# Kernel optimization log

Measured on AMD Instinct MI355X. Metric: run time of the kernel, lower is better.

Reference implementation:

```python
import jax, jax.numpy as jnp
import numpy as np

DIM = 192
HEADS = 6
HIDDEN = 384  # int(DIM * 2.0)


def _ln(x, w, b):
    # WithBias LayerNorm over channel dim (torch normalizes last dim of b,(hw),c)
    mu = jnp.mean(x, axis=1, keepdims=True)
    var = jnp.var(x, axis=1, keepdims=True)
    return (x - mu) / jnp.sqrt(var + 1e-5) * w[None, :, None, None] + b[None, :, None, None]


def _conv1x1(x, w):  # w: [O, I, 1, 1]
    return jnp.einsum('bihw,oi->bohw', x, w[:, :, 0, 0])


def _dwconv3(x, w):  # depthwise 3x3, w: [C, 1, 3, 3]
    return jax.lax.conv_general_dilated(
        x, w, window_strides=(1, 1), padding=((1, 1), (1, 1)),
        feature_group_count=x.shape[1],
        dimension_numbers=('NCHW', 'OIHW', 'NCHW'))


def _l2norm(x):  # F.normalize along last axis
    n = jnp.sqrt(jnp.sum(x * x, axis=-1, keepdims=True))
    return x / jnp.maximum(n, 1e-12)


def setup_inputs() -> dict:
    key = jax.random.key(0)
    ks = jax.random.split(key, 16)
    s = 0.02
    d = {}
    d['x'] = jax.random.normal(ks[0], (2, DIM, 128, 128), dtype=jnp.float32)
    d['k_v'] = jax.random.normal(ks[1], (2, 256), dtype=jnp.float32)
    d['ln1_w'] = jnp.ones((DIM,), jnp.float32)
    d['ln1_b'] = jnp.zeros((DIM,), jnp.float32)
    d['temp'] = jnp.ones((HEADS, 1, 1), jnp.float32)
    d['w_kR'] = jax.random.normal(ks[2], (DIM * 3 // 4, 192), jnp.float32) * s
    d['w_kI'] = jax.random.normal(ks[3], (DIM // 4, 64), jnp.float32) * s
    d['w_qR'] = jax.random.normal(ks[4], (DIM, DIM * 3 // 4, 1, 1), jnp.float32) * s
    d['w_qdw'] = jax.random.normal(ks[5], (DIM, 1, 3, 3), jnp.float32) * s
    d['w_kvI'] = jax.random.normal(ks[6], (DIM * 2, DIM // 4, 1, 1), jnp.float32) * s
    d['w_kvdw'] = jax.random.normal(ks[7], (DIM * 2, 1, 3, 3), jnp.float32) * s
    d['w_po'] = jax.random.normal(ks[8], (DIM, DIM, 1, 1), jnp.float32) * s
    d['ln2_w'] = jnp.ones((DIM,), jnp.float32)
    d['ln2_b'] = jnp.zeros((DIM,), jnp.float32)
    d['w_ffk'] = jax.random.normal(ks[9], (DIM, 256), jnp.float32) * s
    d['w_pin'] = jax.random.normal(ks[10], (HIDDEN * 2, DIM, 1, 1), jnp.float32) * s
    d['w_dw'] = jax.random.normal(ks[11], (HIDDEN * 2, 1, 3, 3), jnp.float32) * s
    d['w_pout'] = jax.random.normal(ks[12], (DIM, HIDDEN, 1, 1), jnp.float32) * s
    return d


def reference(x, k_v, ln1_w, ln1_b, temp, w_kR, w_kI, w_qR, w_qdw, w_kvI, w_kvdw,
              w_po, ln2_w, ln2_b, w_ffk, w_pin, w_dw, w_pout):
    b, c, h, w = x.shape
    c3 = c * 3 // 4
    # ---- Rttention on norm1(x) ----
    xn = _ln(x, ln1_w, ln1_b)
    kvr = (k_v[:, :192] @ w_kR.T)[:, :, None, None]   # [b, 3c/4, 1, 1]
    kvi = (k_v[:, 192:] @ w_kI.T)[:, :, None, None]   # [b, c/4, 1, 1]
    x_r = xn[:, :c3] * kvr + xn[:, :c3]
    x_i = xn[:, c3:] * kvi + xn[:, c3:]
    q = _dwconv3(_conv1x1(x_r, w_qR), w_qdw)          # [b, c, h, w]
    kv = _dwconv3(_conv1x1(x_i, w_kvI), w_kvdw)       # [b, 2c, h, w]
    k, v = jnp.split(kv, 2, axis=1)
    rh = lambda t: t.reshape(b, HEADS, c // HEADS, h * w)
    q = _l2norm(rh(q))
    k = _l2norm(rh(k))
    v = rh(v)
    # channel-wise attention: [b, head, c_h, c_h]
    attn = jax.nn.softmax(jnp.einsum('bhcd,bhed->bhce', q, k) * temp[None], axis=-1)
    out = jnp.einsum('bhce,bhed->bhcd', attn, v).reshape(b, c, h, w)
    x = x + _conv1x1(out, w_po)
    # ---- GDFN FeedForward on norm2(x) ----
    xn2 = _ln(x, ln2_w, ln2_b)
    kvf = (k_v @ w_ffk.T)[:, :, None, None]           # [b, c, 1, 1]
    y = xn2 * kvf + xn2
    y = _dwconv3(_conv1x1(y, w_pin), w_dw)            # [b, 2*hidden, h, w]
    y1, y2 = jnp.split(y, 2, axis=1)
    y = jax.nn.gelu(y1, approximate=False) * y2
    x = x + _conv1x1(y, w_pout)
    return (x, k_v)
```

## Files before the change

kernel.cpp:

```cpp
#include <hip/hip_runtime.h>
#include <math.h>

#define HW 16384
#define IMG 128
#define CDIM 192
#define C3 144
#define C4 48
#define NB 2
#define NPX 32768
#define HEADS 6

typedef unsigned short u16;
typedef unsigned int u32;
typedef __attribute__((ext_vector_type(8))) short bf16x8;
typedef __attribute__((ext_vector_type(4))) float f32x4;

__device__ __forceinline__ float bf2f(u16 u) {
    return __uint_as_float(((unsigned int)u) << 16);
}
__device__ __forceinline__ u16 f2bf(float f) {
    unsigned int x = __float_as_uint(f);
    unsigned int r = x + 0x7fffu + ((x >> 16) & 1u);
    return (u16)(r >> 16);
}

static inline float* wsf(void* ws, size_t off) { return (float*)((char*)ws + off); }
static inline u16* wsh(void* ws, size_t off) { return (u16*)((char*)ws + off); }

__global__ void k_setup(const float* __restrict__ kvv, const float* __restrict__ wkR,
                        const float* __restrict__ wkI, const float* __restrict__ wffk,
                        const float* __restrict__ wqR, const float* __restrict__ wkvI,
                        const float* __restrict__ wpo, const float* __restrict__ wpin,
                        const float* __restrict__ wpout,
                        u16* __restrict__ wb, float* __restrict__ sm,
                        float* __restrict__ tail) {
    int t = blockIdx.x * 256 + threadIdx.x;
    if (t < 313344) {
        float v;
        if (t < 30720) {
            int o = t / 160, i = t % 160;
            v = (i < 144) ? wqR[o * 144 + i] : 0.f;
        } else if (t < 55296) {
            int r = t - 30720; int o = r / 64, i = r % 64;
            v = (i < 48) ? wkvI[o * 48 + i] : 0.f;
        } else if (t < 92160) {
            v = wpo[t - 55296];
        } else if (t < 239616) {
            v = wpin[t - 92160];
        } else {
            v = wpout[t - 239616];
        }
        wb[t] = f2bf(v);
    } else if (t < 314112) {
        int r = t - 313344;
        if (r < 288) {
            int b = r / 144, o = r % 144;
            const float* v = kvv + b * 256;
            const float* w = wkR + o * 192;
            float s = 0.f;
            for (int j = 0; j < 192; j++) s += v[j] * w[j];
            sm[r] = s + 1.0f;
        } else if (r < 384) {
            int r2 = r - 288;
            int b = r2 / 48, o = r2 % 48;
            const float* v = kvv + b * 256 + 192;
            const float* w = wkI + o * 64;
            float s = 0.f;
            for (int j = 0; j < 64; j++) s += v[j] * w[j];
            sm[288 + r2] = s + 1.0f;
        } else {
            int r2 = r - 384;
            int b = r2 / 192, o = r2 % 192;
            const float* v = kvv + b * 256;
            const float* w = wffk + o * 256;
            float s = 0.f;
            for (int j = 0; j < 256; j++) s += v[j] * w[j];
            sm[384 + r2] = s + 1.0f;
        }
    } else if (t < 314624) {
        int r = t - 314112;
        tail[r] = kvv[r];
    }
}

template <bool INBF, bool SPLIT>
__global__ __launch_bounds__(256) void k_ln(
    const void* __restrict__ xin,
    const float* __restrict__ lnw, const float* __restrict__ lnb,
    const float* __restrict__ sca, const float* __restrict__ scb,
    u16* __restrict__ outA, u16* __restrict__ outB) {
    __shared__ float red[2][16][16][4];
    __shared__ float mu_s[16][4], rstd_s[16][4];
    int t = threadIdx.x;
    int px4 = t & 15, cg = t >> 4;
    int base = blockIdx.x * 64;
    int b = base >> 14;
    int p = (base & 16383) + px4 * 4;
    float vals[12][4];
    float s[4] = {0.f, 0.f, 0.f, 0.f}, s2[4] = {0.f, 0.f, 0.f, 0.f};
#pragma unroll
    for (int j = 0; j < 12; j++) {
        int c = cg * 12 + j;
        size_t off = ((size_t)(b * CDIM + c)) * HW + p;
        float v[4];
        if (INBF) {
            ushort4 u = *(const ushort4*)((const u16*)xin + off);
            v[0] = bf2f(u.x); v[1] = bf2f(u.y); v[2] = bf2f(u.z); v[3] = bf2f(u.w);
        } else {
            float4 f = *(const float4*)((const float*)xin + off);
            v[0] = f.x; v[1] = f.y; v[2] = f.z; v[3] = f.w;
        }
#pragma unroll
        for (int q = 0; q < 4; q++) {
            vals[j][q] = v[q]; s[q] += v[q]; s2[q] += v[q] * v[q];
        }
    }
#pragma unroll
    for (int q = 0; q < 4; q++) { red[0][cg][px4][q] = s[q]; red[1][cg][px4][q] = s2[q]; }
    __syncthreads();
    if (t < 16) {
        float S[4] = {0.f, 0.f, 0.f, 0.f}, S2[4] = {0.f, 0.f, 0.f, 0.f};
        for (int g2 = 0; g2 < 16; g2++)
#pragma unroll
            for (int q = 0; q < 4; q++) { S[q] += red[0][g2][t][q]; S2[q] += red[1][g2][t][q]; }
#pragma unroll
        for (int q = 0; q < 4; q++) {
            float mu = S[q] * (1.0f / CDIM);
            float var = S2[q] * (1.0f / CDIM) - mu * mu;
            mu_s[t][q] = mu;
            rstd_s[t][q] = rsqrtf(var + 1e-5f);
        }
    }
    __syncthreads();
    float mu[4], rs[4];
#pragma unroll
    for (int q = 0; q < 4; q++) { mu[q] = mu_s[px4][q]; rs[q] = rstd_s[px4][q]; }
#pragma unroll
    for (int j = 0; j < 12; j++) {
        int c = cg * 12 + j;
        float w = lnw[c], bb = lnb[c];
        float sc; u16* op; size_t off;
        if (SPLIT) {
            if (c < C3) { sc = sca[b * C3 + c]; off = ((size_t)(b * C3 + c)) * HW + p; op = outA; }
            else { sc = scb[b * C4 + c - C3]; off = ((size_t)(b * C4 + c - C3)) * HW + p; op = outB; }
        } else {
            sc = sca[b * CDIM + c]; off = ((size_t)(b * CDIM + c)) * HW + p; op = outA;
        }
        ushort4 o;
        o.x = f2bf(((vals[j][0] - mu[0]) * rs[0] * w + bb) * sc);
        o.y = f2bf(((vals[j][1] - mu[1]) * rs[1] * w + bb) * sc);
        o.z = f2bf(((vals[j][2] - mu[2]) * rs[2] * w + bb) * sc);
        o.w = f2bf(((vals[j][3] - mu[3]) * rs[3] * w + bb) * sc);
        *(ushort4*)(op + off) = o;
    }
}

template <int NCH, int MODE>
__global__ __launch_bounds__(256) void k_gemm(
    const u16* __restrict__ X, int xrows,
    const u16* __restrict__ Wb,
    const void* __restrict__ resid, void* __restrict__ outp, int CO) {
    constexpr int CIP = NCH * 32;
    __shared__ __align__(16) u16 Ws[64 * 32];
    __shared__ __align__(16) u16 Xs[32 * 130];
    const int tid = threadIdx.x;
    const int n0 = blockIdx.x * 128;
    const int m0 = blockIdx.y * 64;
    const int b = blockIdx.z;
    const u16* Xb = X + (size_t)b * xrows * HW + n0;
    const int wave = tid >> 6, lane = tid & 63;
    const int quad = lane >> 4, l16 = lane & 15;
    const int smr = tid >> 2, sk4 = tid & 3;
    const int skr = tid >> 3, sc0 = (tid & 7) * 16;
    f32x4 acc[4][2] = {};
    for (int ch = 0; ch < NCH; ch++) {
        const int k0 = ch * 32;
        if (ch) __syncthreads();
        {
            const int4 wv = *(const int4*)(Wb + (size_t)(m0 + smr) * CIP + k0 + sk4 * 8);
            *(int4*)&Ws[(smr << 5) + (((sk4 ^ (smr & 3)) & 3) << 3)] = wv;
        }
        {
            const u16* xc = Xb + (size_t)(k0 + skr) * HW + sc0;
            int4 r0 = *(const int4*)xc;
            int4 r1 = *(const int4*)(xc + 8);
            u32* dst = (u32*)&Xs[skr * 130 + sc0];
#pragma unroll
            for (int i = 0; i < 4; i++) dst[i] = ((const u32*)&r0)[i];
#pragma unroll
            for (int i = 0; i < 4; i++) dst[4 + i] = ((const u32*)&r1)[i];
        }
        __syncthreads();
        bf16x8 af[4];
#pragma unroll
        for (int mi = 0; mi < 4; mi++) {
            int row = mi * 16 + l16;
            af[mi] = *(const bf16x8*)&Ws[(row << 5) + ((quad ^ (row & 3)) << 3)];
        }
#pragma unroll
        for (int ni = 0; ni < 2; ni++) {
            int n = wave * 32 + ni * 16 + l16;
            bf16x8 bfr;
#pragma unroll
            for (int j = 0; j < 8; j++) bfr[j] = (short)Xs[(quad * 8 + j) * 130 + n];
#pragma unroll
            for (int mi = 0; mi < 4; mi++)
                acc[mi][ni] = __builtin_amdgcn_mfma_f32_16x16x32_bf16(af[mi], bfr, acc[mi][ni], 0, 0, 0);
        }
    }
#pragma unroll
    for (int mi = 0; mi < 4; mi++) {
#pragma unroll
        for (int ni = 0; ni < 2; ni++) {
#pragma unroll
            for (int r = 0; r < 4; r++) {
                int m = m0 + mi * 16 + quad * 4 + r;
                int n = n0 + wave * 32 + ni * 16 + l16;
                size_t idx = ((size_t)b * CO + m) * HW + n;
                float v = acc[mi][ni][r];
                if (MODE == 0) {
                    ((u16*)outp)[idx] = f2bf(v);
                } else if (MODE == 1) {
                    v += ((const float*)resid)[idx];
                    ((u16*)outp)[idx] = f2bf(v);
                } else {
                    v += bf2f(((const u16*)resid)[idx]);
                    ((float*)outp)[idx] = v;
                }
            }
        }
    }
}

__global__ __launch_bounds__(256) void k_dw2(const u16* __restrict__ X,
                                             const float* __restrict__ Wd,
                                             u16* __restrict__ out, int C, int sqCh,
                                             float* __restrict__ sqp) {
    __shared__ float In[34 * 132];
    __shared__ float red[4];
    int bc = blockIdx.x >> 2, rt = blockIdx.x & 3;
    int b = bc / C, ch = bc % C;
    const u16* xb = X + (size_t)bc * HW;
    int t = threadIdx.x;
    int c0 = (t & 7) * 16;
    for (int r = t >> 3; r < 34; r += 32) {
        int y = rt * 32 - 1 + r;
        float* dst = &In[r * 132 + 1 + c0];
        if ((unsigned)y < 128u) {
            const u16* src = xb + y * 128 + c0;
            int4 r0 = *(const int4*)src;
            int4 r1 = *(const int4*)(src + 8);
            const u16* p0 = (const u16*)&r0;
            const u16* p1 = (const u16*)&r1;
#pragma unroll
            for (int i = 0; i < 8; i++) dst[i] = bf2f(p0[i]);
#pragma unroll
            for (int i = 0; i < 8; i++) dst[8 + i] = bf2f(p1[i]);
        } else {
#pragma unroll
            for (int i = 0; i < 16; i++) dst[i] = 0.f;
        }
    }
    if (t < 34) { In[t * 132] = 0.f; In[t * 132 + 129] = 0.f; }
    __syncthreads();
    const float* w = Wd + ch * 9;
    float w00 = w[0], w01 = w[1], w02 = w[2], w10 = w[3], w11 = w[4],
          w12 = w[5], w20 = w[6], w21 = w[7], w22 = w[8];
    int x = t & 127, rg = t >> 7;
    int base = rg * 16;
    float A2 = 0.f, A1 = 0.f, B1 = 0.f, ssq = 0.f;
    u16* ob = out + (size_t)bc * HW + (rt * 32 + base) * 128 + x;
#pragma unroll
    for (int r = 0; r < 18; r++) {
        const float* row = &In[(base + r) * 132 + x];
        float v0 = row[0], v1 = row[1], v2 = row[2];
        float h0 = w00 * v0 + w01 * v1 + w02 * v2;
        float h1 = w10 * v0 + w11 * v1 + w12 * v2;
        float h2 = w20 * v0 + w21 * v1 + w22 * v2;
        if (r >= 2) {
            float val = A2 + B1 + h2;
            ob[(size_t)(r - 2) * 128] = f2bf(val);
            ssq += val * val;
        }
        A2 = A1; A1 = h0; B1 = h1;
    }
    if (ch < sqCh) {
        for (int o = 32; o > 0; o >>= 1) ssq += __shfl_down(ssq, o, 64);
        int wid = t >> 6, lane = t & 63;
        if (lane == 0) red[wid] = ssq;
        __syncthreads();
        if (t == 0) sqp[((b * 192 + ch) << 2) | rt] = red[0] + red[1] + red[2] + red[3];
    }
}

__global__ __launch_bounds__(256) void k_dw_gelu2(const u16* __restrict__ G0,
                                                  const float* __restrict__ Wd,
                                                  u16* __restrict__ out) {
    __shared__ float In[2 * 34 * 132];
    int bc = blockIdx.x >> 2, rt = blockIdx.x & 3;
    int b = bc / 384, j = bc % 384;
    int t = threadIdx.x;
    int c0 = (t & 7) * 16;
    for (int pl = 0; pl < 2; pl++) {
        const u16* xb = G0 + ((size_t)b * 768 + pl * 384 + j) * HW;
        float* pla = &In[pl * 34 * 132];
        for (int r = t >> 3; r < 34; r += 32) {
            int y = rt * 32 - 1 + r;
            float* dst = &pla[r * 132 + 1 + c0];
            if ((unsigned)y < 128u) {
                const u16* src = xb + y * 128 + c0;
                int4 r0 = *(const int4*)src;
                int4 r1 = *(const int4*)(src + 8);
                const u16* p0 = (const u16*)&r0;
                const u16* p1 = (const u16*)&r1;
#pragma unroll
                for (int i = 0; i < 8; i++) dst[i] = bf2f(p0[i]);
#pragma unroll
                for (int i = 0; i < 8; i++) dst[8 + i] = bf2f(p1[i]);
            } else {
#pragma unroll
                for (int i = 0; i < 16; i++) dst[i] = 0.f;
            }
        }
        if (t < 34) { pla[t * 132] = 0.f; pla[t * 132 + 129] = 0.f; }
    }
    __syncthreads();
    const float* w1 = Wd + j * 9;
    const float* w2 = Wd + (384 + j) * 9;
    float a00 = w1[0], a01 = w1[1], a02 = w1[2], a10 = w1[3], a11 = w1[4],
          a12 = w1[5], a20 = w1[6], a21 = w1[7], a22 = w1[8];
    float b00 = w2[0], b01 = w2[1], b02 = w2[2], b10 = w2[3], b11 = w2[4],
          b12 = w2[5], b20 = w2[6], b21 = w2[7], b22 = w2[8];
    int x = t & 127, rg = t >> 7;
    int base = rg * 16;
    float A2a = 0.f, A1a = 0.f, B1a = 0.f;
    float A2b = 0.f, A1b = 0.f, B1b = 0.f;
    u16* ob = out + ((size_t)b * 384 + j) * HW + (rt * 32 + base) * 128 + x;
#pragma unroll
    for (int r = 0; r < 18; r++) {
        const float* r1p = &In[(base + r) * 132 + x];
        const float* r2p = r1p + 34 * 132;
        float u0 = r1p[0], u1 = r1p[1], u2 = r1p[2];
        float v0 = r2p[0], v1 = r2p[1], v2 = r2p[2];
        float h0a = a00 * u0 + a01 * u1 + a02 * u2;
        float h1a = a10 * u0 + a11 * u1 + a12 * u2;
        float h2a = a20 * u0 + a21 * u1 + a22 * u2;
        float h0b = b00 * v0 + b01 * v1 + b02 * v2;
        float h1b = b10 * v0 + b11 * v1 + b12 * v2;
        float h2b = b20 * v0 + b21 * v1 + b22 * v2;
        if (r >= 2) {
            float s1 = A2a + B1a + h2a;
            float s2 = A2b + B1b + h2b;
            float g = 0.5f * s1 * (1.0f + erff(s1 * 0.70710678118654752f));
            ob[(size_t)(r - 2) * 128] = f2bf(g * s2);
        }
        A2a = A1a; A1a = h0a; B1a = h1a;
        A2b = A1b; A1b = h0b; B1b = h1b;
    }
}

__global__ __launch_bounds__(256) void k_qk(const u16* __restrict__ qb_,
                                            const u16* __restrict__ kb_,
                                            float* __restrict__ Spart) {
    int bh = blockIdx.x >> 5, ds = blockIdx.x & 31;
    int b = bh / HEADS, h = bh % HEADS;
    int tid = threadIdx.x;
    int wave = tid >> 6, lane = tid & 63;
    int quad = lane >> 4, l16 = lane & 15;
    int tm = wave >> 1, tn = wave & 1;
    const u16* qrow = qb_ + ((size_t)(b * 192 + h * 32 + tm * 16 + l16)) * HW + ds * 512 + quad * 8;
    const u16* krow = kb_ + ((size_t)(b * 384 + h * 32 + tn * 16 + l16)) * HW + ds * 512 + quad * 8;
    f32x4 acc = {};
#pragma unroll
    for (int ch = 0; ch < 16; ch++) {
        bf16x8 a = *(const bf16x8*)(qrow + ch * 32);
        bf16x8 k8 = *(const bf16x8*)(krow + ch * 32);
        acc = __builtin_amdgcn_mfma_f32_16x16x32_bf16(a, k8, acc, 0, 0, 0);
    }
    float* Sb = Spart + ((size_t)ds * 12 + bh) * 1024;
#pragma unroll
    for (int r = 0; r < 4; r++)
        Sb[(tm * 16 + quad * 4 + r) * 32 + tn * 16 + l16] = acc[r];
}

__global__ void k_softmax(const float* __restrict__ Spart, const float* __restrict__ sqqp,
                          const float* __restrict__ sqkp, const float* __restrict__ temp,
                          u16* __restrict__ attnb) {
    int row = blockIdx.x;
    int bh = row >> 5, c2 = row & 31;
    int b = bh / HEADS, h = bh % HEADS;
    int e = threadIdx.x;
    float l = -1e30f;
    if (e < 32) {
        float s = 0.f;
        for (int d = 0; d < 32; d++) s += Spart[((size_t)d * 12 + bh) * 1024 + c2 * 32 + e];
        const float* qp = sqqp + (b * 192 + h * 32 + c2) * 4;
        const float* kp = sqkp + (b * 192 + h * 32 + e) * 4;
        float nq = qp[0] + qp[1] + qp[2] + qp[3];
        float nk = kp[0] + kp[1] + kp[2] + kp[3];
        float invq = 1.0f / fmaxf(sqrtf(nq), 1e-12f);
        float invk = 1.0f / fmaxf(sqrtf(nk), 1e-12f);
        l = s * invq * invk * temp[h];
    }
    float m = l;
    for (int o = 32; o > 0; o >>= 1) m = fmaxf(m, __shfl_xor(m, o, 64));
    float ev = (e < 32) ? expf(l - m) : 0.f;
    float ssum = ev;
    for (int o = 32; o > 0; o >>= 1) ssum += __shfl_xor(ssum, o, 64);
    if (e < 32) attnb[bh * 1024 + c2 * 32 + e] = f2bf(ev / ssum);
}

__global__ __launch_bounds__(256) void k_av(const u16* __restrict__ attnb,
                                            const u16* __restrict__ kvb,
                                            u16* __restrict__ out) {
    __shared__ __align__(16) u16 Vs[32 * 130];
    int bh = blockIdx.x >> 7;
    int pt = blockIdx.x & 127;
    int b = bh / HEADS, h = bh % HEADS;
    int p0 = pt * 128;
    int t = threadIdx.x;
    {
        int e = t >> 3, c0 = (t & 7) * 16;
        const u16* src = kvb + ((size_t)(b * 384 + 192 + h * 32 + e)) * HW + p0 + c0;
        int4 r0 = *(const int4*)src;
        int4 r1 = *(const int4*)(src + 8);
        u32* dst = (u32*)&Vs[e * 130 + c0];
#pragma unroll
        for (int i = 0; i < 4; i++) dst[i] = ((const u32*)&r0)[i];
#pragma unroll
        for (int i = 0; i < 4; i++) dst[4 + i] = ((const u32*)&r1)[i];
    }
    __syncthreads();
    int wave = t >> 6, lane = t & 63;
    int quad = lane >> 4, l16 = lane & 15;
    f32x4 acc[2][2] = {};
    bf16x8 af[2];
#pragma unroll
    for (int tm = 0; tm < 2; tm++)
        af[tm] = *(const bf16x8*)(attnb + bh * 1024 + (tm * 16 + l16) * 32 + quad * 8);
#pragma unroll
    for (int nt = 0; nt < 2; nt++) {
        int n = wave * 32 + nt * 16 + l16;
        bf16x8 bfr;
#pragma unroll
        for (int j = 0; j < 8; j++) bfr[j] = (short)Vs[(quad * 8 + j) * 130 + n];
#pragma unroll
        for (int tm = 0; tm < 2; tm++)
            acc[tm][nt] = __builtin_amdgcn_mfma_f32_16x16x32_bf16(af[tm], bfr, acc[tm][nt], 0, 0, 0);
    }
#pragma unroll
    for (int tm = 0; tm < 2; tm++)
#pragma unroll
        for (int nt = 0; nt < 2; nt++)
#pragma unroll
            for (int r = 0; r < 4; r++) {
                int c = h * 32 + tm * 16 + quad * 4 + r;
                int p = p0 + wave * 32 + nt * 16 + l16;
                out[((size_t)b * 192 + c) * HW + p] = f2bf(acc[tm][nt][r]);
            }
}

extern "C" void kernel_launch(void* const* d_in, const int* in_sizes, int n_in,
                              void* d_out, int out_size, void* d_ws, size_t ws_size,
                              hipStream_t stream) {
    const float* x     = (const float*)d_in[0];
    const float* k_v   = (const float*)d_in[1];
    const float* ln1w  = (const float*)d_in[2];
    const float* ln1b  = (const float*)d_in[3];
    const float* temp  = (const float*)d_in[4];
    const float* w_kR  = (const float*)d_in[5];
    const float* w_kI  = (const float*)d_in[6];
    const float* w_qR  = (const float*)d_in[7];
    const float* w_qdw = (const float*)d_in[8];
    const float* w_kvI = (const float*)d_in[9];
    const float* w_kvdw= (const float*)d_in[10];
    const float* w_po  = (const float*)d_in[11];
    const float* ln2w  = (const float*)d_in[12];
    const float* ln2b  = (const float*)d_in[13];
    const float* w_ffk = (const float*)d_in[14];
    const float* w_pin = (const float*)d_in[15];
    const float* w_dw  = (const float*)d_in[16];
    const float* w_pout= (const float*)d_in[17];
    float* out = (float*)d_out;

    const size_t MiB = 1048576ULL;
    u16*   q0b     = wsh(d_ws, 0);
    u16*   attnoutb= wsh(d_ws, 0);
    u16*   y0b     = wsh(d_ws, 0);
    u16*   kv0b    = wsh(d_ws, 12 * MiB);
    u16*   ybufb   = wsh(d_ws, 12 * MiB);
    u16*   x1b     = wsh(d_ws, 36 * MiB);
    u16*   qbuf_b  = wsh(d_ws, 48 * MiB);
    u16*   kvbuf_b = wsh(d_ws, 60 * MiB);
    u16*   xrb     = wsh(d_ws, 84 * MiB);
    u16*   xib     = wsh(d_ws, 94 * MiB);
    u16*   g0b     = wsh(d_ws, 98 * MiB);
    u16*   wb      = wsh(d_ws, 146 * MiB);
    float* sm      = wsf(d_ws, 147 * MiB);
    float* Spart   = wsf(d_ws, 148 * MiB);
    u16* wq   = wb;
    u16* wkv  = wb + 30720;
    u16* wpo  = wb + 55296;
    u16* wpin = wb + 92160;
    u16* wpout= wb + 239616;
    float* kvr  = sm;
    float* kvi  = sm + 288;
    float* kvf  = sm + 384;
    float* sqqp = sm + 768;
    float* sqkp = sm + 2304;
    u16*   attnb= (u16*)(sm + 3840);

    k_setup<<<1229, 256, 0, stream>>>(k_v, w_kR, w_kI, w_ffk, w_qR, w_kvI, w_po,
                                      w_pin, w_pout, wb, sm,
                                      out + (size_t)NB * CDIM * HW);
    k_ln<false, true><<<NPX / 64, 256, 0, stream>>>(x, ln1w, ln1b, kvr, kvi, xrb, xib);
    k_gemm<5, 0><<<dim3(128, 3, 2), 256, 0, stream>>>(xrb, 144, wq, nullptr, q0b, 192);
    k_gemm<2, 0><<<dim3(128, 6, 2), 256, 0, stream>>>(xib, 48, wkv, nullptr, kv0b, 384);
    k_dw2<<<NB * 192 * 4, 256, 0, stream>>>(q0b, w_qdw, qbuf_b, 192, 192, sqqp);
    k_dw2<<<NB * 384 * 4, 256, 0, stream>>>(kv0b, w_kvdw, kvbuf_b, 384, 192, sqkp);
    k_qk<<<12 * 32, 256, 0, stream>>>(qbuf_b, kvbuf_b, Spart);
    k_softmax<<<384, 64, 0, stream>>>(Spart, sqqp, sqkp, temp, attnb);
    k_av<<<12 * 128, 256, 0, stream>>>(attnb, kvbuf_b, attnoutb);
    k_gemm<6, 1><<<dim3(128, 3, 2), 256, 0, stream>>>(attnoutb, 192, wpo, x, x1b, 192);
    k_ln<true, false><<<NPX / 64, 256, 0, stream>>>(x1b, ln2w, ln2b, kvf, nullptr, y0b, nullptr);
    k_gemm<6, 0><<<dim3(128, 12, 2), 256, 0, stream>>>(y0b, 192, wpin, nullptr, g0b, 768);
    k_dw_gelu2<<<NB * 384 * 4, 256, 0, stream>>>(g0b, w_dw, ybufb);
    k_gemm<12, 2><<<dim3(128, 3, 2), 256, 0, stream>>>(ybufb, 384, wpout, x1b, out, 192);
}
```

Before: 269.2 us.

## Store GEMM inputs pixel-major so MFMA operands load directly without LDS

```diff
diff --git a/kernel.cpp b/kernel.cpp
--- a/kernel.cpp
+++ b/kernel.cpp
@@ -2,7 +2,6 @@
 #include <math.h>
 
 #define HW 16384
-#define IMG 128
 #define CDIM 192
 #define C3 144
 #define C4 48
@@ -32,7 +31,9 @@
                         const float* __restrict__ wqR, const float* __restrict__ wkvI,
                         const float* __restrict__ wpo, const float* __restrict__ wpin,
                         const float* __restrict__ wpout,
+                        const float* __restrict__ ln2w, const float* __restrict__ ln2b,
                         u16* __restrict__ wb, float* __restrict__ sm,
+                        float* __restrict__ A2, float* __restrict__ B2,
                         float* __restrict__ tail) {
     int t = blockIdx.x * 256 + threadIdx.x;
     if (t < 313344) {
@@ -75,7 +76,10 @@
             const float* w = wffk + o * 256;
             float s = 0.f;
             for (int j = 0; j < 256; j++) s += v[j] * w[j];
-            sm[384 + r2] = s + 1.0f;
+            float sc = s + 1.0f;
+            sm[384 + r2] = sc;
+            A2[r2] = ln2w[o] * sc;
+            B2[r2] = ln2b[o] * sc;
         }
     } else if (t < 314624) {
         int r = t - 314112;
@@ -83,9 +87,8 @@
     }
 }
 
-template <bool INBF, bool SPLIT>
-__global__ __launch_bounds__(256) void k_ln(
-    const void* __restrict__ xin,
+__global__ __launch_bounds__(256) void k_ln1(
+    const float* __restrict__ xin,
     const float* __restrict__ lnw, const float* __restrict__ lnb,
     const float* __restrict__ sca, const float* __restrict__ scb,
     u16* __restrict__ outA, u16* __restrict__ outB) {
@@ -102,14 +105,8 @@
     for (int j = 0; j < 12; j++) {
         int c = cg * 12 + j;
         size_t off = ((size_t)(b * CDIM + c)) * HW + p;
-        float v[4];
-        if (INBF) {
-            ushort4 u = *(const ushort4*)((const u16*)xin + off);
-            v[0] = bf2f(u.x); v[1] = bf2f(u.y); v[2] = bf2f(u.z); v[3] = bf2f(u.w);
-        } else {
-            float4 f = *(const float4*)((const float*)xin + off);
-            v[0] = f.x; v[1] = f.y; v[2] = f.z; v[3] = f.w;
-        }
+        float4 f = *(const float4*)(xin + off);
+        float v[4] = {f.x, f.y, f.z, f.w};
 #pragma unroll
         for (int q = 0; q < 4; q++) {
             vals[j][q] = v[q]; s[q] += v[q]; s2[q] += v[q] * v[q];
@@ -135,31 +132,101 @@
     float mu[4], rs[4];
 #pragma unroll
     for (int q = 0; q < 4; q++) { mu[q] = mu_s[px4][q]; rs[q] = rstd_s[px4][q]; }
+    float Ac[12], Bc[12];
 #pragma unroll
     for (int j = 0; j < 12; j++) {
         int c = cg * 12 + j;
-        float w = lnw[c], bb = lnb[c];
-        float sc; u16* op; size_t off;
-        if (SPLIT) {
-            if (c < C3) { sc = sca[b * C3 + c]; off = ((size_t)(b * C3 + c)) * HW + p; op = outA; }
-            else { sc = scb[b * C4 + c - C3]; off = ((size_t)(b * C4 + c - C3)) * HW + p; op = outB; }
-        } else {
-            sc = sca[b * CDIM + c]; off = ((size_t)(b * CDIM + c)) * HW + p; op = outA;
-        }
-        ushort4 o;
-        o.x = f2bf(((vals[j][0] - mu[0]) * rs[0] * w + bb) * sc);
-        o.y = f2bf(((vals[j][1] - mu[1]) * rs[1] * w + bb) * sc);
-        o.z = f2bf(((vals[j][2] - mu[2]) * rs[2] * w + bb) * sc);
-        o.w = f2bf(((vals[j][3] - mu[3]) * rs[3] * w + bb) * sc);
-        *(ushort4*)(op + off) = o;
+        float sc = (c < C3) ? sca[b * C3 + c] : scb[b * C4 + (c - C3)];
+        Ac[j] = lnw[c] * sc;
+        Bc[j] = lnb[c] * sc;
+    }
+    int isR = (cg < 12);
+    size_t row0 = (size_t)b * HW + p;
+    u16* basep = isR ? (outA + row0 * 160 + cg * 12)
+                     : (outB + row0 * 64 + (cg * 12 - 144));
+    int rowlen = isR ? 160 : 64;
+#pragma unroll
+    for (int q = 0; q < 4; q++) {
+        u16 tmp[12];
+#pragma unroll
+        for (int j = 0; j < 12; j++)
+            tmp[j] = f2bf((vals[j][q] - mu[q]) * rs[q] * Ac[j] + Bc[j]);
+        u16* op = basep + q * rowlen;
+        ushort4 o0 = {tmp[0], tmp[1], tmp[2], tmp[3]};
+        ushort4 o1 = {tmp[4], tmp[5], tmp[6], tmp[7]};
+        ushort4 o2 = {tmp[8], tmp[9], tmp[10], tmp[11]};
+        *(ushort4*)(op) = o0;
+        *(ushort4*)(op + 4) = o1;
+        *(ushort4*)(op + 8) = o2;
+    }
+    if (cg == 0) {
+        int4 z = {0, 0, 0, 0};
+#pragma unroll
+        for (int q = 0; q < 4; q++) {
+            u16* pr = outA + (row0 + q) * 160 + 144;
+            *(int4*)(pr) = z; *(int4*)(pr + 8) = z;
+            u16* pi = outB + (row0 + q) * 64 + 48;
+            *(int4*)(pi) = z; *(int4*)(pi + 8) = z;
+        }
     }
 }
 
 template <int NCH, int MODE>
-__global__ __launch_bounds__(256) void k_gemm(
-    const u16* __restrict__ X, int xrows,
-    const u16* __restrict__ Wb,
+__global__ __launch_bounds__(256) void k_gemm_t(
+    const u16* __restrict__ X, const u16* __restrict__ Wb,
     const void* __restrict__ resid, void* __restrict__ outp, int CO) {
+    constexpr int CIP = NCH * 32;
+    const int tid = threadIdx.x;
+    const int n0 = blockIdx.x * 128;
+    const int m0 = blockIdx.y * 64;
+    const int b = blockIdx.z;
+    const int wave = tid >> 6, lane = tid & 63;
+    const int quad = lane >> 4, l16 = lane & 15;
+    const u16* arow = Wb + (size_t)(m0 + l16) * CIP + quad * 8;
+    const u16* brow = X + ((size_t)b * HW + n0 + wave * 32 + l16) * CIP + quad * 8;
+    f32x4 acc[4][2] = {};
+#pragma unroll
+    for (int ch = 0; ch < NCH; ch++) {
+        const int k0 = ch * 32;
+        bf16x8 bf0 = *(const bf16x8*)(brow + k0);
+        bf16x8 bf1 = *(const bf16x8*)(brow + 16 * CIP + k0);
+        bf16x8 af[4];
+#pragma unroll
+        for (int mi = 0; mi < 4; mi++)
+            af[mi] = *(const bf16x8*)(arow + mi * 16 * CIP + k0);
+#pragma unroll
+        for (int mi = 0; mi < 4; mi++) {
+            acc[mi][0] = __builtin_amdgcn_mfma_f32_16x16x32_bf16(af[mi], bf0, acc[mi][0], 0, 0, 0);
+            acc[mi][1] = __builtin_amdgcn_mfma_f32_16x16x32_bf16(af[mi], bf1, acc[mi][1], 0, 0, 0);
+        }
+    }
+#pragma unroll
+    for (int mi = 0; mi < 4; mi++) {
+#pragma unroll
+        for (int ni = 0; ni < 2; ni++) {
+            int c0 = m0 + mi * 16 + quad * 4;
+            int px = n0 + wave * 32 + ni * 16 + l16;
+            if (MODE == 0) {
+                u16* ob = (u16*)outp + ((size_t)b * CO + c0) * HW + px;
+#pragma unroll
+                for (int r = 0; r < 4; r++) ob[(size_t)r * HW] = f2bf(acc[mi][ni][r]);
+            } else {
+                const float* rp = (const float*)resid + ((size_t)b * 192 + c0) * HW + px;
+                ushort4 o;
+                o.x = f2bf(acc[mi][ni][0] + rp[0]);
+                o.y = f2bf(acc[mi][ni][1] + rp[(size_t)HW]);
+                o.z = f2bf(acc[mi][ni][2] + rp[(size_t)2 * HW]);
+                o.w = f2bf(acc[mi][ni][3] + rp[(size_t)3 * HW]);
+                *(ushort4*)((u16*)outp + ((size_t)b * HW + px) * 192 + c0) = o;
+            }
+        }
+    }
+}
+
+__global__ __launch_bounds__(256) void k_gemm_s(
+    const u16* __restrict__ X, const u16* __restrict__ Wb,
+    const u16* __restrict__ residT, float* __restrict__ outp) {
+    constexpr int NCH = 12;
     constexpr int CIP = NCH * 32;
     __shared__ __align__(16) u16 Ws[64 * 32];
     __shared__ __align__(16) u16 Xs[32 * 130];
@@ -167,7 +234,7 @@
     const int n0 = blockIdx.x * 128;
     const int m0 = blockIdx.y * 64;
     const int b = blockIdx.z;
-    const u16* Xb = X + (size_t)b * xrows * HW + n0;
+    const u16* Xb = X + (size_t)b * 384 * HW + n0;
     const int wave = tid >> 6, lane = tid & 63;
     const int quad = lane >> 4, l16 = lane & 15;
     const int smr = tid >> 2, sk4 = tid & 3;
@@ -212,22 +279,14 @@
     for (int mi = 0; mi < 4; mi++) {
 #pragma unroll
         for (int ni = 0; ni < 2; ni++) {
-#pragma unroll
-            for (int r = 0; r < 4; r++) {
-                int m = m0 + mi * 16 + quad * 4 + r;
-                int n = n0 + wave * 32 + ni * 16 + l16;
-                size_t idx = ((size_t)b * CO + m) * HW + n;
-                float v = acc[mi][ni][r];
-                if (MODE == 0) {
-                    ((u16*)outp)[idx] = f2bf(v);
-                } else if (MODE == 1) {
-                    v += ((const float*)resid)[idx];
-                    ((u16*)outp)[idx] = f2bf(v);
-                } else {
-                    v += bf2f(((const u16*)resid)[idx]);
-                    ((float*)outp)[idx] = v;
-                }
-            }
+            int c0 = m0 + mi * 16 + quad * 4;
+            int px = n0 + wave * 32 + ni * 16 + l16;
+            ushort4 rv = *(const ushort4*)(residT + ((size_t)b * HW + px) * 192 + c0);
+            float* ob = outp + ((size_t)b * 192 + c0) * HW + px;
+            ob[0] = acc[mi][ni][0] + bf2f(rv.x);
+            ob[(size_t)HW] = acc[mi][ni][1] + bf2f(rv.y);
+            ob[(size_t)2 * HW] = acc[mi][ni][2] + bf2f(rv.z);
+            ob[(size_t)3 * HW] = acc[mi][ni][3] + bf2f(rv.w);
         }
     }
 }
@@ -451,13 +510,56 @@
 #pragma unroll
     for (int tm = 0; tm < 2; tm++)
 #pragma unroll
-        for (int nt = 0; nt < 2; nt++)
-#pragma unroll
-            for (int r = 0; r < 4; r++) {
-                int c = h * 32 + tm * 16 + quad * 4 + r;
-                int p = p0 + wave * 32 + nt * 16 + l16;
-                out[((size_t)b * 192 + c) * HW + p] = f2bf(acc[tm][nt][r]);
-            }
+        for (int nt = 0; nt < 2; nt++) {
+            int c0 = h * 32 + tm * 16 + quad * 4;
+            int px = p0 + wave * 32 + nt * 16 + l16;
+            ushort4 o;
+            o.x = f2bf(acc[tm][nt][0]);
+            o.y = f2bf(acc[tm][nt][1]);
+            o.z = f2bf(acc[tm][nt][2]);
+            o.w = f2bf(acc[tm][nt][3]);
+            *(ushort4*)(out + ((size_t)b * HW + px) * 192 + c0) = o;
+        }
+}
+
+__global__ __launch_bounds__(256) void k_ln2t(
+    const u16* __restrict__ xin, const float* __restrict__ A2,
+    const float* __restrict__ B2, u16* __restrict__ outp) {
+    int t = threadIdx.x;
+    int pxg = blockIdx.x * 64 + (t >> 2);
+    int l2 = t & 3;
+    int b = pxg >> 14;
+    const u16* src = xin + (size_t)pxg * 192 + l2 * 48;
+    float v[48];
+    float s = 0.f, s2 = 0.f;
+#pragma unroll
+    for (int i = 0; i < 6; i++) {
+        int4 r0 = *(const int4*)(src + i * 8);
+        const u16* pp = (const u16*)&r0;
+#pragma unroll
+        for (int k = 0; k < 8; k++) {
+            float f = bf2f(pp[k]);
+            v[i * 8 + k] = f; s += f; s2 += f * f;
+        }
+    }
+    s += __shfl_xor(s, 1, 64);  s += __shfl_xor(s, 2, 64);
+    s2 += __shfl_xor(s2, 1, 64); s2 += __shfl_xor(s2, 2, 64);
+    float mu = s * (1.0f / CDIM);
+    float rstd = rsqrtf(s2 * (1.0f / CDIM) - mu * mu + 1e-5f);
+    const float* Ap = A2 + b * 192 + l2 * 48;
+    const float* Bp = B2 + b * 192 + l2 * 48;
+    u16* dst = outp + (size_t)pxg * 192 + l2 * 48;
+#pragma unroll
+    for (int i = 0; i < 12; i++) {
+        float4 a = *(const float4*)(Ap + i * 4);
+        float4 bb = *(const float4*)(Bp + i * 4);
+        ushort4 o;
+        o.x = f2bf((v[i * 4 + 0] - mu) * rstd * a.x + bb.x);
+        o.y = f2bf((v[i * 4 + 1] - mu) * rstd * a.y + bb.y);
+        o.z = f2bf((v[i * 4 + 2] - mu) * rstd * a.z + bb.z);
+        o.w = f2bf((v[i * 4 + 3] - mu) * rstd * a.w + bb.w);
+        *(ushort4*)(dst + i * 4) = o;
+    }
 }
 
 extern "C" void kernel_launch(void* const* d_in, const int* in_sizes, int n_in,
@@ -505,25 +607,26 @@
     u16* wpout= wb + 239616;
     float* kvr  = sm;
     float* kvi  = sm + 288;
-    float* kvf  = sm + 384;
     float* sqqp = sm + 768;
     float* sqkp = sm + 2304;
     u16*   attnb= (u16*)(sm + 3840);
+    float* A2c  = sm + 10240;
+    float* B2c  = sm + 10624;
 
     k_setup<<<1229, 256, 0, stream>>>(k_v, w_kR, w_kI, w_ffk, w_qR, w_kvI, w_po,
-                                      w_pin, w_pout, wb, sm,
+                                      w_pin, w_pout, ln2w, ln2b, wb, sm, A2c, B2c,
                                       out + (size_t)NB * CDIM * HW);
-    k_ln<false, true><<<NPX / 64, 256, 0, stream>>>(x, ln1w, ln1b, kvr, kvi, xrb, xib);
-    k_gemm<5, 0><<<dim3(128, 3, 2), 256, 0, stream>>>(xrb, 144, wq, nullptr, q0b, 192);
-    k_gemm<2, 0><<<dim3(128, 6, 2), 256, 0, stream>>>(xib, 48, wkv, nullptr, kv0b, 384);
+    k_ln1<<<NPX / 64, 256, 0, stream>>>(x, ln1w, ln1b, kvr, kvi, xrb, xib);
+    k_gemm_t<5, 0><<<dim3(128, 3, 2), 256, 0, stream>>>(xrb, wq, nullptr, q0b, 192);
+    k_gemm_t<2, 0><<<dim3(128, 6, 2), 256, 0, stream>>>(xib, wkv, nullptr, kv0b, 384);
     k_dw2<<<NB * 192 * 4, 256, 0, stream>>>(q0b, w_qdw, qbuf_b, 192, 192, sqqp);
     k_dw2<<<NB * 384 * 4, 256, 0, stream>>>(kv0b, w_kvdw, kvbuf_b, 384, 192, sqkp);
     k_qk<<<12 * 32, 256, 0, stream>>>(qbuf_b, kvbuf_b, Spart);
     k_softmax<<<384, 64, 0, stream>>>(Spart, sqqp, sqkp, temp, attnb);
     k_av<<<12 * 128, 256, 0, stream>>>(attnb, kvbuf_b, attnoutb);
-    k_gemm<6, 1><<<dim3(128, 3, 2), 256, 0, stream>>>(attnoutb, 192, wpo, x, x1b, 192);
-    k_ln<true, false><<<NPX / 64, 256, 0, stream>>>(x1b, ln2w, ln2b, kvf, nullptr, y0b, nullptr);
-    k_gemm<6, 0><<<dim3(128, 12, 2), 256, 0, stream>>>(y0b, 192, wpin, nullptr, g0b, 768);
+    k_gemm_t<6, 1><<<dim3(128, 3, 2), 256, 0, stream>>>(attnoutb, wpo, x, x1b, 192);
+    k_ln2t<<<NPX / 64, 256, 0, stream>>>(x1b, A2c, B2c, y0b);
+    k_gemm_t<6, 0><<<dim3(128, 12, 2), 256, 0, stream>>>(y0b, wpin, nullptr, g0b, 768);
     k_dw_gelu2<<<NB * 384 * 4, 256, 0, stream>>>(g0b, w_dw, ybufb);
-    k_gemm<12, 2><<<dim3(128, 3, 2), 256, 0, stream>>>(ybufb, 384, wpout, x1b, out, 192);
-}
+    k_gemm_s<<<dim3(128, 3, 2), 256, 0, stream>>>(ybufb, wpout, x1b, out);
+}
```

Result: slower. 306.7 us (+13.9%).
